# Kernel optimization log

Hardware: AMD Instinct MI355X
Metric: run time of the kernel (lower is better)

## Reference

```python
import jax, jax.numpy as jnp
import numpy as np

N = 256        # num_nodes
F = 256        # feature_dim
B = 32         # batch
DEG = 32       # out-degree per node -> E = N*DEG edges


def setup_inputs() -> dict:
    key = jax.random.key(0)
    k1, k2, k3, k4 = jax.random.split(key, 4)
    node_features = jax.random.normal(k1, (B, N, F), dtype=jnp.float32)
    # xavier_uniform for [N, N, F] tensor: fan_in = N*F, fan_out = N*F per torch default flattening
    limit = float(np.sqrt(6.0 / (N * F + N * F)))
    W = jax.random.uniform(k2, (N, N, F), dtype=jnp.float32, minval=-limit, maxval=limit)
    phase = jax.random.uniform(k3, (N, N), dtype=jnp.float32, minval=0.0, maxval=2.0 * np.pi)
    # topology: each node i has DEG outgoing connections (paths[i])
    src = jnp.repeat(jnp.arange(N, dtype=jnp.int64), DEG)              # [E]
    dst = jax.random.randint(k4, (N * DEG,), 0, N, dtype=jnp.int64)    # [E]
    return {"node_features": node_features, "W": W, "phase": phase, "src": src, "dst": dst}


def reference(node_features, W, phase, src, dst):
    # real(exp(i*phase)) == cos(phase); per-edge effective weight [E, F]
    eff_w = W[src, dst, :] * jnp.cos(phase[src, dst])[:, None]
    # gather source node features and scale: [B, E, F]
    signal = node_features[:, src, :] * eff_w[None, :, :]
    # scatter-add into destination nodes
    propagated = jnp.zeros_like(node_features).at[:, dst, :].add(signal)
    # normalization by out-degree of each node index (matches original indexing)
    n = node_features.shape[1]
    counts = jnp.zeros((n,), dtype=node_features.dtype).at[src].add(1.0)
    norm = jnp.maximum(counts, 1.0)
    return propagated / norm[None, :, None]
```

## Files before the change

kernel.cpp:

```cpp
#include <hip/hip_runtime.h>
#include <math.h>

#define NN 256
#define FF 256
#define BB 32
#define EE 8192

#define BGROUPS 2
#define CAP 1024

__device__ __forceinline__ void fma4(float4& a, const float4 x, const float4 w) {
    a.x = fmaf(x.x, w.x, a.x);
    a.y = fmaf(x.y, w.y, a.y);
    a.z = fmaf(x.z, w.z, a.z);
    a.w = fmaf(x.w, w.w, a.w);
}

__global__ __launch_bounds__(256) void fused_propagate_kernel(
    const float4* __restrict__ nf4,
    const float4* __restrict__ W4,
    const float*  __restrict__ phase,
    const int*    __restrict__ src,
    const int*    __restrict__ dst,
    float4*       __restrict__ out4)
{
    const int d     = blockIdx.x;
    const int tid   = threadIdx.x;
    const int tf    = tid & 63;
    const int bsub  = tid >> 6;
    const int bbase = blockIdx.y * (BB / BGROUPS) + bsub * 4;

    __shared__ int   ls[CAP];
    __shared__ float lc[CAP];
    __shared__ int   s_cnt;
    __shared__ int   s_srccnt;
    __shared__ int   s_n;

    if (tid == 0) { s_cnt = 0; s_srccnt = 0; }
    __syncthreads();

    const int4* dst4 = (const int4*)dst;
    const int4* src4 = (const int4*)src;
    int mysrc = 0;
    for (int i = tid; i < EE / 4; i += 256) {
        const int4 dv = dst4[i];
        const int4 sv = src4[i];
        if (dv.x == d) { int p = atomicAdd(&s_cnt, 1); if (p < CAP) { ls[p] = sv.x; lc[p] = cosf(phase[sv.x * NN + d]); } }
        if (dv.y == d) { int p = atomicAdd(&s_cnt, 1); if (p < CAP) { ls[p] = sv.y; lc[p] = cosf(phase[sv.y * NN + d]); } }
        if (dv.z == d) { int p = atomicAdd(&s_cnt, 1); if (p < CAP) { ls[p] = sv.z; lc[p] = cosf(phase[sv.z * NN + d]); } }
        if (dv.w == d) { int p = atomicAdd(&s_cnt, 1); if (p < CAP) { ls[p] = sv.w; lc[p] = cosf(phase[sv.w * NN + d]); } }
        mysrc += (sv.x == d) + (sv.y == d) + (sv.z == d) + (sv.w == d);
    }
    if (mysrc) atomicAdd(&s_srccnt, mysrc);
    __syncthreads();

    if (tid == 0) {
        int n  = min(s_cnt, CAP);
        int n4 = (n + 3) & ~3;
        for (int i = n; i < n4; i++) { ls[i] = 0; lc[i] = 0.0f; }
        s_n = n4;
    }
    __syncthreads();

    const int   nlist = s_n;
    const float rn    = 1.0f / fmaxf((float)s_srccnt, 1.0f);

    float4 acc0 = {0.f, 0.f, 0.f, 0.f};
    float4 acc1 = {0.f, 0.f, 0.f, 0.f};
    float4 acc2 = {0.f, 0.f, 0.f, 0.f};
    float4 acc3 = {0.f, 0.f, 0.f, 0.f};

    const int woff = d * (FF / 4) + tf;
    const int nfo0 = (bbase + 0) * NN * (FF / 4) + tf;
    const int nfo1 = (bbase + 1) * NN * (FF / 4) + tf;
    const int nfo2 = (bbase + 2) * NN * (FF / 4) + tf;
    const int nfo3 = (bbase + 3) * NN * (FF / 4) + tf;

    for (int k = 0; k < nlist; k += 4) {
        const int   s0 = ls[k + 0], s1 = ls[k + 1], s2 = ls[k + 2], s3 = ls[k + 3];
        const float c0 = lc[k + 0], c1 = lc[k + 1], c2 = lc[k + 2], c3 = lc[k + 3];

        float4 w0 = W4[s0 * (NN * FF / 4) + woff];
        float4 w1 = W4[s1 * (NN * FF / 4) + woff];
        float4 w2 = W4[s2 * (NN * FF / 4) + woff];
        float4 w3 = W4[s3 * (NN * FF / 4) + woff];

        const float4 x00 = nf4[nfo0 + s0 * (FF / 4)];
        const float4 x01 = nf4[nfo1 + s0 * (FF / 4)];
        const float4 x02 = nf4[nfo2 + s0 * (FF / 4)];
        const float4 x03 = nf4[nfo3 + s0 * (FF / 4)];
        const float4 x10 = nf4[nfo0 + s1 * (FF / 4)];
        const float4 x11 = nf4[nfo1 + s1 * (FF / 4)];
        const float4 x12 = nf4[nfo2 + s1 * (FF / 4)];
        const float4 x13 = nf4[nfo3 + s1 * (FF / 4)];
        const float4 x20 = nf4[nfo0 + s2 * (FF / 4)];
        const float4 x21 = nf4[nfo1 + s2 * (FF / 4)];
        const float4 x22 = nf4[nfo2 + s2 * (FF / 4)];
        const float4 x23 = nf4[nfo3 + s2 * (FF / 4)];
        const float4 x30 = nf4[nfo0 + s3 * (FF / 4)];
        const float4 x31 = nf4[nfo1 + s3 * (FF / 4)];
        const float4 x32 = nf4[nfo2 + s3 * (FF / 4)];
        const float4 x33 = nf4[nfo3 + s3 * (FF / 4)];

        w0.x *= c0; w0.y *= c0; w0.z *= c0; w0.w *= c0;
        w1.x *= c1; w1.y *= c1; w1.z *= c1; w1.w *= c1;
        w2.x *= c2; w2.y *= c2; w2.z *= c2; w2.w *= c2;
        w3.x *= c3; w3.y *= c3; w3.z *= c3; w3.w *= c3;

        fma4(acc0, x00, w0); fma4(acc1, x01, w0); fma4(acc2, x02, w0); fma4(acc3, x03, w0);
        fma4(acc0, x10, w1); fma4(acc1, x11, w1); fma4(acc2, x12, w1); fma4(acc3, x13, w1);
        fma4(acc0, x20, w2); fma4(acc1, x21, w2); fma4(acc2, x22, w2); fma4(acc3, x23, w2);
        fma4(acc0, x30, w3); fma4(acc1, x31, w3); fma4(acc2, x32, w3); fma4(acc3, x33, w3);
    }

    const int oo = d * (FF / 4) + tf;
    float4 o;
    o.x = acc0.x * rn; o.y = acc0.y * rn; o.z = acc0.z * rn; o.w = acc0.w * rn;
    out4[(bbase + 0) * NN * (FF / 4) + oo] = o;
    o.x = acc1.x * rn; o.y = acc1.y * rn; o.z = acc1.z * rn; o.w = acc1.w * rn;
    out4[(bbase + 1) * NN * (FF / 4) + oo] = o;
    o.x = acc2.x * rn; o.y = acc2.y * rn; o.z = acc2.z * rn; o.w = acc2.w * rn;
    out4[(bbase + 2) * NN * (FF / 4) + oo] = o;
    o.x = acc3.x * rn; o.y = acc3.y * rn; o.z = acc3.z * rn; o.w = acc3.w * rn;
    out4[(bbase + 3) * NN * (FF / 4) + oo] = o;
}

extern "C" void kernel_launch(void* const* d_in, const int* in_sizes, int n_in,
                              void* d_out, int out_size, void* d_ws, size_t ws_size,
                              hipStream_t stream) {
    const float* nf    = (const float*)d_in[0];
    const float* W     = (const float*)d_in[1];
    const float* phase = (const float*)d_in[2];
    const int*   src   = (const int*)d_in[3];
    const int*   dst   = (const int*)d_in[4];
    float*       out   = (float*)d_out;

    dim3 grid(NN, BGROUPS);
    fused_propagate_kernel<<<grid, 256, 0, stream>>>(
        (const float4*)nf, (const float4*)W, phase, src, dst, (float4*)out);
}
```

Baseline: 127.7 us.

## Split blocks by feature slice and build edge list with prefix scan

Blocks now split over feature quarters instead of batch halves, so each block covers all 32 batches and every W row slice is gathered once rather than once per batch group. Each thread keeps two batch accumulators instead of four, which lowers register pressure but also lowers per-thread load parallelism. The shared-memory atomic edge-list build is replaced by a two-pass count plus block prefix scan, giving a deterministic, ordered list without atomic contention. The CAP bound check on the list is dropped.

```diff
diff --git a/kernel.cpp b/kernel.cpp
--- a/kernel.cpp
+++ b/kernel.cpp
@@ -6,8 +6,9 @@
 #define BB 32
 #define EE 8192
 
-#define BGROUPS 2
+#define FGROUPS 4
 #define CAP 1024
+#define EPT (EE / 4 / 256)
 
 __device__ __forceinline__ void fma4(float4& a, const float4 x, const float4 w) {
     a.x = fmaf(x.x, w.x, a.x);
@@ -24,105 +25,97 @@
     const int*    __restrict__ dst,
     float4*       __restrict__ out4)
 {
-    const int d     = blockIdx.x;
-    const int tid   = threadIdx.x;
-    const int tf    = tid & 63;
-    const int bsub  = tid >> 6;
-    const int bbase = blockIdx.y * (BB / BGROUPS) + bsub * 4;
+    const int d   = blockIdx.x;
+    const int tid = threadIdx.x;
+    const int f4  = blockIdx.y * (FF / 4 / FGROUPS) + (tid & 15);
+    const int b0  = (tid >> 4) * 2;
 
     __shared__ int   ls[CAP];
     __shared__ float lc[CAP];
-    __shared__ int   s_cnt;
-    __shared__ int   s_srccnt;
-    __shared__ int   s_n;
-
-    if (tid == 0) { s_cnt = 0; s_srccnt = 0; }
-    __syncthreads();
+    __shared__ int   sc[256];
 
     const int4* dst4 = (const int4*)dst;
     const int4* src4 = (const int4*)src;
-    int mysrc = 0;
-    for (int i = tid; i < EE / 4; i += 256) {
-        const int4 dv = dst4[i];
-        const int4 sv = src4[i];
-        if (dv.x == d) { int p = atomicAdd(&s_cnt, 1); if (p < CAP) { ls[p] = sv.x; lc[p] = cosf(phase[sv.x * NN + d]); } }
-        if (dv.y == d) { int p = atomicAdd(&s_cnt, 1); if (p < CAP) { ls[p] = sv.y; lc[p] = cosf(phase[sv.y * NN + d]); } }
-        if (dv.z == d) { int p = atomicAdd(&s_cnt, 1); if (p < CAP) { ls[p] = sv.z; lc[p] = cosf(phase[sv.z * NN + d]); } }
-        if (dv.w == d) { int p = atomicAdd(&s_cnt, 1); if (p < CAP) { ls[p] = sv.w; lc[p] = cosf(phase[sv.w * NN + d]); } }
-        mysrc += (sv.x == d) + (sv.y == d) + (sv.z == d) + (sv.w == d);
+    const int   i0   = tid * EPT;
+
+    int cnt = 0, msrc = 0;
+    for (int i = 0; i < EPT; i++) {
+        const int4 dv = dst4[i0 + i];
+        const int4 sv = src4[i0 + i];
+        cnt  += (dv.x == d) + (dv.y == d) + (dv.z == d) + (dv.w == d);
+        msrc += (sv.x == d) + (sv.y == d) + (sv.z == d) + (sv.w == d);
     }
-    if (mysrc) atomicAdd(&s_srccnt, mysrc);
+
+    sc[tid] = cnt | (msrc << 16);
+    __syncthreads();
+    for (int off = 1; off < 256; off <<= 1) {
+        int v = 0;
+        if (tid >= off) v = sc[tid - off];
+        __syncthreads();
+        if (tid >= off) sc[tid] += v;
+        __syncthreads();
+    }
+    const int totals = sc[255];
+    const int n      = totals & 0xFFFF;
+    const int srccnt = totals >> 16;
+    int base = (sc[tid] & 0xFFFF) - cnt;
+
+    for (int i = 0; i < EPT; i++) {
+        const int4 dv = dst4[i0 + i];
+        const int4 sv = src4[i0 + i];
+        if (dv.x == d) { ls[base] = sv.x; lc[base] = cosf(phase[sv.x * NN + d]); base++; }
+        if (dv.y == d) { ls[base] = sv.y; lc[base] = cosf(phase[sv.y * NN + d]); base++; }
+        if (dv.z == d) { ls[base] = sv.z; lc[base] = cosf(phase[sv.z * NN + d]); base++; }
+        if (dv.w == d) { ls[base] = sv.w; lc[base] = cosf(phase[sv.w * NN + d]); base++; }
+    }
+    const int n4 = (n + 3) & ~3;
+    if (tid < n4 - n) { ls[n + tid] = 0; lc[n + tid] = 0.0f; }
     __syncthreads();
 
-    if (tid == 0) {
-        int n  = min(s_cnt, CAP);
-        int n4 = (n + 3) & ~3;
-        for (int i = n; i < n4; i++) { ls[i] = 0; lc[i] = 0.0f; }
-        s_n = n4;
-    }
-    __syncthreads();
-
-    const int   nlist = s_n;
-    const float rn    = 1.0f / fmaxf((float)s_srccnt, 1.0f);
+    const float rn = 1.0f / fmaxf((float)srccnt, 1.0f);
 
     float4 acc0 = {0.f, 0.f, 0.f, 0.f};
     float4 acc1 = {0.f, 0.f, 0.f, 0.f};
-    float4 acc2 = {0.f, 0.f, 0.f, 0.f};
-    float4 acc3 = {0.f, 0.f, 0.f, 0.f};
 
-    const int woff = d * (FF / 4) + tf;
-    const int nfo0 = (bbase + 0) * NN * (FF / 4) + tf;
-    const int nfo1 = (bbase + 1) * NN * (FF / 4) + tf;
-    const int nfo2 = (bbase + 2) * NN * (FF / 4) + tf;
-    const int nfo3 = (bbase + 3) * NN * (FF / 4) + tf;
+    const int wdf = d * (FF / 4) + f4;
+    const int nb0 = (b0 + 0) * NN * (FF / 4) + f4;
+    const int nb1 = (b0 + 1) * NN * (FF / 4) + f4;
 
-    for (int k = 0; k < nlist; k += 4) {
+    for (int k = 0; k < n4; k += 4) {
         const int   s0 = ls[k + 0], s1 = ls[k + 1], s2 = ls[k + 2], s3 = ls[k + 3];
         const float c0 = lc[k + 0], c1 = lc[k + 1], c2 = lc[k + 2], c3 = lc[k + 3];
 
-        float4 w0 = W4[s0 * (NN * FF / 4) + woff];
-        float4 w1 = W4[s1 * (NN * FF / 4) + woff];
-        float4 w2 = W4[s2 * (NN * FF / 4) + woff];
-        float4 w3 = W4[s3 * (NN * FF / 4) + woff];
+        float4 w0 = W4[s0 * (NN * FF / 4) + wdf];
+        float4 w1 = W4[s1 * (NN * FF / 4) + wdf];
+        float4 w2 = W4[s2 * (NN * FF / 4) + wdf];
+        float4 w3 = W4[s3 * (NN * FF / 4) + wdf];
 
-        const float4 x00 = nf4[nfo0 + s0 * (FF / 4)];
-        const float4 x01 = nf4[nfo1 + s0 * (FF / 4)];
-        const float4 x02 = nf4[nfo2 + s0 * (FF / 4)];
-        const float4 x03 = nf4[nfo3 + s0 * (FF / 4)];
-        const float4 x10 = nf4[nfo0 + s1 * (FF / 4)];
-        const float4 x11 = nf4[nfo1 + s1 * (FF / 4)];
-        const float4 x12 = nf4[nfo2 + s1 * (FF / 4)];
-        const float4 x13 = nf4[nfo3 + s1 * (FF / 4)];
-        const float4 x20 = nf4[nfo0 + s2 * (FF / 4)];
-        const float4 x21 = nf4[nfo1 + s2 * (FF / 4)];
-        const float4 x22 = nf4[nfo2 + s2 * (FF / 4)];
-        const float4 x23 = nf4[nfo3 + s2 * (FF / 4)];
-        const float4 x30 = nf4[nfo0 + s3 * (FF / 4)];
-        const float4 x31 = nf4[nfo1 + s3 * (FF / 4)];
-        const float4 x32 = nf4[nfo2 + s3 * (FF / 4)];
-        const float4 x33 = nf4[nfo3 + s3 * (FF / 4)];
+        const float4 x00 = nf4[nb0 + s0 * (FF / 4)];
+        const float4 x01 = nf4[nb1 + s0 * (FF / 4)];
+        const float4 x10 = nf4[nb0 + s1 * (FF / 4)];
+        const float4 x11 = nf4[nb1 + s1 * (FF / 4)];
+        const float4 x20 = nf4[nb0 + s2 * (FF / 4)];
+        const float4 x21 = nf4[nb1 + s2 * (FF / 4)];
+        const float4 x30 = nf4[nb0 + s3 * (FF / 4)];
+        const float4 x31 = nf4[nb1 + s3 * (FF / 4)];
 
         w0.x *= c0; w0.y *= c0; w0.z *= c0; w0.w *= c0;
         w1.x *= c1; w1.y *= c1; w1.z *= c1; w1.w *= c1;
         w2.x *= c2; w2.y *= c2; w2.z *= c2; w2.w *= c2;
         w3.x *= c3; w3.y *= c3; w3.z *= c3; w3.w *= c3;
 
-        fma4(acc0, x00, w0); fma4(acc1, x01, w0); fma4(acc2, x02, w0); fma4(acc3, x03, w0);
-        fma4(acc0, x10, w1); fma4(acc1, x11, w1); fma4(acc2, x12, w1); fma4(acc3, x13, w1);
-        fma4(acc0, x20, w2); fma4(acc1, x21, w2); fma4(acc2, x22, w2); fma4(acc3, x23, w2);
-        fma4(acc0, x30, w3); fma4(acc1, x31, w3); fma4(acc2, x32, w3); fma4(acc3, x33, w3);
+        fma4(acc0, x00, w0); fma4(acc1, x01, w0);
+        fma4(acc0, x10, w1); fma4(acc1, x11, w1);
+        fma4(acc0, x20, w2); fma4(acc1, x21, w2);
+        fma4(acc0, x30, w3); fma4(acc1, x31, w3);
     }
 
-    const int oo = d * (FF / 4) + tf;
+    const int od = d * (FF / 4) + f4;
     float4 o;
     o.x = acc0.x * rn; o.y = acc0.y * rn; o.z = acc0.z * rn; o.w = acc0.w * rn;
-    out4[(bbase + 0) * NN * (FF / 4) + oo] = o;
+    out4[(b0 + 0) * NN * (FF / 4) + od] = o;
     o.x = acc1.x * rn; o.y = acc1.y * rn; o.z = acc1.z * rn; o.w = acc1.w * rn;
-    out4[(bbase + 1) * NN * (FF / 4) + oo] = o;
-    o.x = acc2.x * rn; o.y = acc2.y * rn; o.z = acc2.z * rn; o.w = acc2.w * rn;
-    out4[(bbase + 2) * NN * (FF / 4) + oo] = o;
-    o.x = acc3.x * rn; o.y = acc3.y * rn; o.z = acc3.z * rn; o.w = acc3.w * rn;
-    out4[(bbase + 3) * NN * (FF / 4) + oo] = o;
+    out4[(b0 + 1) * NN * (FF / 4) + od] = o;
 }
 
 extern "C" void kernel_launch(void* const* d_in, const int* in_sizes, int n_in,
@@ -135,7 +128,7 @@
     const int*   dst   = (const int*)d_in[4];
     float*       out   = (float*)d_out;
 
-    dim3 grid(NN, BGROUPS);
+    dim3 grid(NN, FGROUPS);
     fused_propagate_kernel<<<grid, 256, 0, stream>>>(
         (const float4*)nf, (const float4*)W, phase, src, dst, (float4*)out);
 }
```

New measurement: 140.4 us. 1.1x slower.
